# Performance work log

Hardware: AMD Instinct MI355X
Metric: run time of the kernel (lower is better)

Reference implementation:

```python
import jax, jax.numpy as jnp
import numpy as np

N = 100000   # nodes
E = 1600000  # message-passing edges (avg degree 16)
ES = 500000  # scored edges (edge_subgraph)
H = 64       # hidden_features
L = 3        # num_layers
NF = 2       # node_features
EF = 2       # edge_features


def setup_inputs() -> dict:
    key = jax.random.key(0)
    ks = jax.random.split(key, 20)
    s = lambda fan_in: 1.0 / np.sqrt(fan_in)
    inp = {
        "x": jax.random.normal(ks[0], (N, NF), jnp.float32),
        "e": jax.random.normal(ks[1], (E, EF), jnp.float32),
        # encoder linears
        "Wn": jax.random.normal(ks[2], (NF, H), jnp.float32) * s(NF),
        "bn": jnp.zeros((H,), jnp.float32),
        "We": jax.random.normal(ks[3], (EF, H), jnp.float32) * s(EF),
        "be": jnp.zeros((H,), jnp.float32),
        # GatedGCN per-layer weights (stacked over L layers)
        # e' = h_src@A + h_dst@B + e@C + cb ; h' = h@U + sum(sig(e')*h_src@V)/sum(sig(e'))
        "A": jax.random.normal(ks[4], (L, H, H), jnp.float32) * s(H),
        "B": jax.random.normal(ks[5], (L, H, H), jnp.float32) * s(H),
        "C": jax.random.normal(ks[6], (L, H, H), jnp.float32) * s(H),
        "cb": jnp.zeros((L, H), jnp.float32),
        "U": jax.random.normal(ks[7], (L, H, H), jnp.float32) * s(H),
        "V": jax.random.normal(ks[8], (L, H, H), jnp.float32) * s(H),
        # score predictor: Linear(2H, 1)
        "Wp": jax.random.normal(ks[9], (2 * H, 1), jnp.float32) * s(2 * H),
        "bp": jnp.zeros((1,), jnp.float32),
        # graph structure
        "src": jax.random.randint(ks[10], (E,), 0, N, jnp.int32),
        "dst": jax.random.randint(ks[11], (E,), 0, N, jnp.int32),
        "src_s": jax.random.randint(ks[12], (ES,), 0, N, jnp.int32),
        "dst_s": jax.random.randint(ks[13], (ES,), 0, N, jnp.int32),
    }
    return inp


def reference(x, e, Wn, bn, We, be, A, B, C, cb, U, V, Wp, bp, src, dst, src_s, dst_s):
    n = x.shape[0]
    h = x @ Wn + bn          # node encode [N, H]
    e = e @ We + be          # edge encode [E, H]
    for i in range(A.shape[0]):  # fixed small layer loop
        hs = h[src]          # gather src feats [E, H]
        hd = h[dst]          # gather dst feats [E, H]
        e_hat = hs @ A[i] + hd @ B[i] + e @ C[i] + cb[i]
        sigma = jax.nn.sigmoid(e_hat)
        num = jax.ops.segment_sum(sigma * (hs @ V[i]), dst, num_segments=n)
        den = jax.ops.segment_sum(sigma, dst, num_segments=n) + 1e-6
        h = jax.nn.relu(h @ U[i] + num / den)
        e = jax.nn.relu(e_hat)
    # apply_edges: gather-concat-linear on scored edge set
    data = jnp.concatenate([h[src_s], h[dst_s]], axis=1)  # [ES, 2H]
    scores = data @ Wp + bp                               # [ES, 1]
    return scores
```

## Files before the change

### kernel.cpp

```cpp
#include <hip/hip_runtime.h>
#include <hip/hip_bf16.h>

using bf16 = __hip_bfloat16;
typedef __attribute__((ext_vector_type(8))) short short8;
typedef __attribute__((ext_vector_type(4))) float f32x4;
typedef __attribute__((ext_vector_type(4))) int   iv4;

static constexpr int NN = 100000;
static constexpr int NE = 1600000;
static constexpr int NS = 500000;
static constexpr int HH = 64;
static constexpr int SCAN_B = 1024;
static constexpr int SCAN_G = (NN + SCAN_B - 1) / SCAN_B;
static constexpr int DPW = 8;
static constexpr int NGRP = (NN + DPW - 1) / DPW;

__device__ __forceinline__ float b2f(bf16 v) { return __bfloat162float(v); }
__device__ __forceinline__ bf16  f2b(float v) { return __float2bfloat16(v); }
__device__ __forceinline__ float bflo(int u)  { return __uint_as_float(((unsigned)u) << 16); }
__device__ __forceinline__ float bfhi(int u)  { return __uint_as_float(((unsigned)u) & 0xffff0000u); }
__device__ __forceinline__ int pk2(float a, float b) {
    unsigned lo = __bfloat16_as_ushort(__float2bfloat16(a));
    unsigned hi = __bfloat16_as_ushort(__float2bfloat16(b));
    return (int)(lo | (hi << 16));
}
__device__ __forceinline__ int bcasti(int v, int k) {
    return __builtin_amdgcn_readlane(v, k);
}


__global__ void encode_nodes_k(const float* __restrict__ x, const float* __restrict__ Wn,
                               const float* __restrict__ bn, float* __restrict__ h) {
    int tid = blockIdx.x * blockDim.x + threadIdx.x;
    if (tid >= NN * HH) return;
    int r = tid >> 6, j = tid & 63;
    h[tid] = fmaf(x[2 * r], Wn[j], fmaf(x[2 * r + 1], Wn[HH + j], bn[j]));
}

__global__ void prep_k(const float* __restrict__ We, const float* __restrict__ be,
                       const float* __restrict__ C0, const float* __restrict__ cb0,
                       float* __restrict__ We0, float* __restrict__ bb0) {
    int j = threadIdx.x;
    if (j >= HH) return;
    float s0 = 0.f, s1 = 0.f, sb = 0.f;
    for (int k = 0; k < HH; ++k) {
        float c = C0[k * HH + j];
        s0 = fmaf(We[k], c, s0);
        s1 = fmaf(We[HH + k], c, s1);
        sb = fmaf(be[k], c, sb);
    }
    We0[j] = s0; We0[HH + j] = s1; bb0[j] = sb + cb0[j];
}


__global__ void zero_int_k(int* __restrict__ p, int n) {
    int i = blockIdx.x * blockDim.x + threadIdx.x;
    if (i < n) p[i] = 0;
}

__global__ void hist_k(const int* __restrict__ dst, int* __restrict__ cnt) {
    int i = blockIdx.x * blockDim.x + threadIdx.x;
    if (i < NE) atomicAdd(&cnt[dst[i]], 1);
}

__global__ void scan1_k(const int* __restrict__ cnt, int* __restrict__ rowptr,
                        int* __restrict__ bsum) {
    __shared__ int sm[SCAN_B];
    int t = threadIdx.x, idx = blockIdx.x * SCAN_B + t;
    int v = (idx < NN) ? cnt[idx] : 0;
    sm[t] = v;
    __syncthreads();
    for (int off = 1; off < SCAN_B; off <<= 1) {
        int add = (t >= off) ? sm[t - off] : 0;
        __syncthreads();
        sm[t] += add;
        __syncthreads();
    }
    if (idx < NN) rowptr[idx] = sm[t] - v;
    if (t == SCAN_B - 1) bsum[blockIdx.x] = sm[t];
}

__global__ void scan2_k(const int* __restrict__ bsum, int* __restrict__ bofs) {
    if (threadIdx.x == 0) {
        int acc = 0;
        for (int b = 0; b < SCAN_G; ++b) { bofs[b] = acc; acc += bsum[b]; }
    }
}

__global__ void scan3_k(int* __restrict__ rowptr, int* __restrict__ cursor,
                        const int* __restrict__ bofs) {
    int idx = blockIdx.x * SCAN_B + threadIdx.x;
    if (idx < NN) {
        int r = rowptr[idx] + bofs[blockIdx.x];
        rowptr[idx] = r;
        cursor[idx] = r;
    }
    if (idx == 0) rowptr[NN] = NE;
}

__global__ void scatter_k(const int* __restrict__ dst, const int* __restrict__ src,
                          const float2* __restrict__ e0, int* __restrict__ cursor,
                          int4* __restrict__ sedge) {
    int i = blockIdx.x * blockDim.x + threadIdx.x;
    if (i < NE) {
        int p = atomicAdd(&cursor[dst[i]], 1);
        float2 ev = e0[i];
        sedge[p] = make_int4(src[i], __float_as_int(ev.x), __float_as_int(ev.y), 0);
    }
}

__global__ __launch_bounds__(256, 2)
void transform_mfma_k(const float* __restrict__ h,
                      const float* __restrict__ A, const float* __restrict__ B,
                      const float* __restrict__ V, const float* __restrict__ U,
                      bf16* __restrict__ oA, bf16* __restrict__ oB,
                      bf16* __restrict__ oV, bf16* __restrict__ oU) {
    __shared__ __align__(16) char lds_all[4 * 2048];
    char* lds = lds_all + (threadIdx.x >> 6) * 2048;
    const int lane = threadIdx.x & 63;
    const int l15 = lane & 15, lg = lane >> 4, kb = lg * 8;
    const float *W0, *W1; bf16 *o0, *o1;
    if (blockIdx.y == 0) { W0 = A; W1 = B; o0 = oA; o1 = oB; }
    else                 { W0 = V; W1 = U; o0 = oV; o1 = oU; }

    short8 wf[2][4][2];
#pragma unroll
    for (int m = 0; m < 2; ++m) {
        const float* W = m ? W1 : W0;
#pragma unroll
        for (int t = 0; t < 4; ++t)
#pragma unroll
            for (int f = 0; f < 2; ++f) {
                iv4 q;
#pragma unroll
                for (int j = 0; j < 4; ++j)
                    q[j] = pk2(W[(f * 32 + kb + 2 * j) * HH + t * 16 + l15],
                               W[(f * 32 + kb + 2 * j + 1) * HH + t * 16 + l15]);
                __builtin_memcpy(&wf[m][t][f], &q, 16);
            }
    }
    const int sw = (l15 & 7) << 4;
    int wave = blockIdx.x * 4 + (threadIdx.x >> 6);
    int nw = gridDim.x * 4;
    for (int tile = wave; tile < NN / 16; tile += nw) {
        int row0 = tile * 16;
        const float* hr = h + (size_t)(row0 + l15) * HH + kb;
        float4 v0 = *(const float4*)(hr);
        float4 v1 = *(const float4*)(hr + 4);
        float4 v2 = *(const float4*)(hr + 32);
        float4 v3 = *(const float4*)(hr + 36);
        iv4 pa, pb;
        pa[0] = pk2(v0.x, v0.y); pa[1] = pk2(v0.z, v0.w);
        pa[2] = pk2(v1.x, v1.y); pa[3] = pk2(v1.z, v1.w);
        pb[0] = pk2(v2.x, v2.y); pb[1] = pk2(v2.z, v2.w);
        pb[2] = pk2(v3.x, v3.y); pb[3] = pk2(v3.z, v3.w);
        short8 af0, af1;
        __builtin_memcpy(&af0, &pa, 16);
        __builtin_memcpy(&af1, &pb, 16);
#pragma unroll
        for (int m = 0; m < 2; ++m) {
            f32x4 acc[4];
#pragma unroll
            for (int t = 0; t < 4; ++t) acc[t] = f32x4{0.f, 0.f, 0.f, 0.f};
#pragma unroll
            for (int t = 0; t < 4; ++t) {
                acc[t] = __builtin_amdgcn_mfma_f32_16x16x32_bf16(af0, wf[m][t][0], acc[t], 0, 0, 0);
                acc[t] = __builtin_amdgcn_mfma_f32_16x16x32_bf16(af1, wf[m][t][1], acc[t], 0, 0, 0);
            }
#pragma unroll
            for (int t = 0; t < 4; ++t)
#pragma unroll
                for (int r = 0; r < 4; ++r) {
                    int row = lg * 4 + r;
                    int ad = (row * 128 + (t * 16 + l15) * 2) ^ ((row & 7) << 4);
                    *(unsigned short*)(lds + ad) =
                        __bfloat16_as_ushort(__float2bfloat16(acc[t][r]));
                }
            int base = l15 * 128 + lg * 32;
            iv4 q0, q1;
            __builtin_memcpy(&q0, lds + ((base) ^ sw), 16);
            __builtin_memcpy(&q1, lds + ((base + 16) ^ sw), 16);
            bf16* out = m ? o1 : o0;
            *(iv4*)(out + (size_t)(row0 + l15) * HH + lg * 16) = q0;
            *(iv4*)(out + (size_t)(row0 + l15) * HH + lg * 16 + 8) = q1;
        }
    }
}

__global__ __launch_bounds__(256, 2)
void agg0_k(float* __restrict__ h, const bf16* __restrict__ tabs,
            const float* __restrict__ We0, const float* __restrict__ bb0,
            const int* __restrict__ rowptr, const int4* __restrict__ sedge) {
    __shared__ float fl_all[4][128];
    float* fl = fl_all[threadIdx.x >> 6];
    const int lane = threadIdx.x & 63;
    const int l15 = lane & 15, lg = lane >> 4;
    const int f0 = l15 * 4;
    const size_t nb = (size_t)NN * HH;

    float w0f[4], w1f[4], bbf[4];
#pragma unroll
    for (int q = 0; q < 4; ++q) {
        w0f[q] = We0[f0 + q];
        w1f[q] = We0[HH + f0 + q];
        bbf[q] = bb0[f0 + q];
    }

    struct R0 { uint2 a0[4], hv[4]; };
    const int nwaves = gridDim.x * 4;
    for (int g = blockIdx.x * 4 + (threadIdx.x >> 6); g < NGRP; g += nwaves) {
        int dA = g * DPW;
        int ndst = min(DPW, NN - dA);
        int rpv = rowptr[dA + min(lane, ndst)];

        auto endof = [&](int i2) { return bcasti(rpv, i2 + 1); };
        auto begof = [&](int i2) { return bcasti(rpv, i2); };
        auto ldsed = [&](int i2, int b2) -> int4 {
            int en = endof(i2);
            int idx = b2 + min(l15, en - b2 - 1);
            return sedge[idx];
        };
        auto ldrows = [&](const int4& sd, R0& R) {
#pragma unroll
            for (int r = 0; r < 4; ++r) {
                int s = __shfl(sd.x, lg + 4 * r);
                R.a0[r] = *(const uint2*)(tabs + (size_t)s * HH + f0);
                R.hv[r] = *(const uint2*)(tabs + 6 * nb + (size_t)s * HH + f0);
            }
        };
        auto succ = [&](int& i2, int& b2) {
            if (i2 >= ndst) return;
            if (b2 + 16 < endof(i2)) { b2 += 16; return; }
            i2++;
            while (i2 < ndst && endof(i2) <= begof(i2)) i2++;
            if (i2 < ndst) b2 = begof(i2);
        };

        int iC = 0;
        while (iC < ndst && endof(iC) <= begof(iC)) iC++;
        int bC = (iC < ndst) ? begof(iC) : 0;
        int4 sedC = make_int4(0, 0, 0, 0), sedN = sedC;
        R0 rowsC, rowsN;
        if (iC < ndst) sedC = ldsed(iC, bC);
        int iN = iC, bN = bC;
        if (iC < ndst) succ(iN, bN);
        if (iN < ndst) sedN = ldsed(iN, bN);
        if (iC < ndst) ldrows(sedC, rowsC);

        for (int i = 0; i < ndst; ++i) {
            size_t drow = (size_t)(dA + i) * HH;
            float hu = b2f(tabs[7 * nb + drow + lane]);
            float zb[4];
            {
                uint2 bv = *(const uint2*)(tabs + nb + drow + f0);
                zb[0] = bbf[0] + bflo(bv.x); zb[1] = bbf[1] + bfhi(bv.x);
                zb[2] = bbf[2] + bflo(bv.y); zb[3] = bbf[3] + bfhi(bv.y);
            }
            float nm[4] = {0.f, 0.f, 0.f, 0.f}, dn[4] = {0.f, 0.f, 0.f, 0.f};

            while (iC == i) {
                if (iN < ndst) ldrows(sedN, rowsN);
                int iF = iN, bF = bN;
                succ(iF, bF);
                int4 sedF = sedN;
                if (iF < ndst) sedF = ldsed(iF, bF);

                int cnt = min(endof(i) - bC, 16);
#pragma unroll
                for (int r = 0; r < 4; ++r) {
                    int s = lg + 4 * r;
                    bool valid = s < cnt;
                    float ex = __int_as_float(__shfl(sedC.y, s));
                    float ey = __int_as_float(__shfl(sedC.z, s));
                    uint2 a0 = rowsC.a0[r], hv = rowsC.hv[r];
                    float av[4] = {bflo(a0.x), bfhi(a0.x), bflo(a0.y), bfhi(a0.y)};
                    float hvv[4] = {bflo(hv.x), bfhi(hv.x), bflo(hv.y), bfhi(hv.y)};
#pragma unroll
                    for (int q = 0; q < 4; ++q) {
                        float z = fmaf(ex, w0f[q], fmaf(ey, w1f[q], zb[q])) + av[q];
                        float sg = valid ? 1.f / (1.f + __expf(-z)) : 0.f;
                        nm[q] = fmaf(sg, hvv[q], nm[q]);
                        dn[q] += sg;
                    }
                }
                sedC = sedN; rowsC = rowsN; iC = iN; bC = bN;
                iN = iF; bN = bF; sedN = sedF;
            }

#pragma unroll
            for (int m = 16; m < 64; m <<= 1)
#pragma unroll
                for (int q = 0; q < 4; ++q) {
                    nm[q] += __shfl_xor(nm[q], m);
                    dn[q] += __shfl_xor(dn[q], m);
                }
            if (lg == 0) {
#pragma unroll
                for (int q = 0; q < 4; ++q) {
                    fl[f0 + q] = nm[q];
                    fl[64 + f0 + q] = dn[q];
                }
            }
            float nmv = fl[lane], dnv = fl[64 + lane];
            h[drow + lane] = fmaxf(hu + nmv / (dnv + 1e-6f), 0.f);
        }
    }
}

struct Rows { iv4 ra, rb, hva, hvb, b1a, b1b, b2a, b2b; };

template <int LAYER>
__global__ __launch_bounds__(256, 2)
void agg_k(float* __restrict__ h, const bf16* __restrict__ tabs,
           const float* __restrict__ We0, const float* __restrict__ bb0,
           const float* __restrict__ cb, const float* __restrict__ C,
           const int* __restrict__ rowptr, const int4* __restrict__ sedge) {
    __shared__ __align__(16) char cfr[LAYER >= 2 ? 16384 : 8192];
    constexpr int WLDS = (LAYER == 1 ? 4096 : 6144);
    __shared__ __align__(16) char lds_all[4 * WLDS];
    char* lds = lds_all + (threadIdx.x >> 6) * WLDS;
    char* Lb1 = lds;
    char* Lb2 = lds + 2048;
    char* Lhv = lds + (LAYER >= 2 ? 4096 : 2048);
    char* Le1 = lds;
    const int lane = threadIdx.x & 63;
    const int l15 = lane & 15, lg = lane >> 4, kb = lg * 8;
    const size_t nb = (size_t)NN * HH;

    {
        int t = threadIdx.x >> 6;
        const float* C1 = C + 1 * HH * HH;
        const float* C2 = C + 2 * HH * HH;
#pragma unroll
        for (int f = 0; f < 2; ++f) {
            iv4 q;
#pragma unroll
            for (int j = 0; j < 4; ++j)
                q[j] = pk2(C1[(f * 32 + kb + 2 * j) * HH + t * 16 + l15],
                           C1[(f * 32 + kb + 2 * j + 1) * HH + t * 16 + l15]);
            *(iv4*)(cfr + ((t * 2 + f) * 64 + lane) * 16) = q;
            if constexpr (LAYER >= 2) {
                iv4 p;
#pragma unroll
                for (int j = 0; j < 4; ++j)
                    p[j] = pk2(C2[(f * 32 + kb + 2 * j) * HH + t * 16 + l15],
                               C2[(f * 32 + kb + 2 * j + 1) * HH + t * 16 + l15]);
                *(iv4*)(cfr + 8192 + ((t * 2 + f) * 64 + lane) * 16) = p;
            }
        }
        __syncthreads();
    }

    float w0a[8], w0b[8], w1a[8], w1b[8], bba[8], bbb[8];
#pragma unroll
    for (int j = 0; j < 8; ++j) {
        w0a[j] = We0[kb + j];        w0b[j] = We0[32 + kb + j];
        w1a[j] = We0[HH + kb + j];   w1b[j] = We0[HH + 32 + kb + j];
        bba[j] = bb0[kb + j];        bbb[j] = bb0[32 + kb + j];
    }
    float cb1t[4], cb2t[4];
#pragma unroll
    for (int t = 0; t < 4; ++t) cb1t[t] = cb[HH + t * 16 + l15];
    if constexpr (LAYER >= 2) {
#pragma unroll
        for (int t = 0; t < 4; ++t) cb2t[t] = cb[2 * HH + t * 16 + l15];
    }
    const int wlo = (l15 * 128 + lg * 16) ^ ((l15 & 7) << 4);
    const int whi = (l15 * 128 + 64 + lg * 16) ^ ((l15 & 7) << 4);

    const int nwaves = gridDim.x * 4;
    for (int g = blockIdx.x * 4 + (threadIdx.x >> 6); g < NGRP; g += nwaves) {
        int dA = g * DPW;
        int ndst = min(DPW, NN - dA);
        int rpv = rowptr[dA + min(lane, ndst)];

        auto endof = [&](int i2) { return bcasti(rpv, i2 + 1); };
        auto begof = [&](int i2) { return bcasti(rpv, i2); };
        auto ldsed = [&](int i2, int b2) -> int4 {
            int en = endof(i2);
            int idx = b2 + min(l15, en - b2 - 1);
            return sedge[idx];
        };
        auto ldrows = [&](const int4& sd, Rows& R) {
            size_t srow = (size_t)sd.x * HH;
            R.ra  = *(const iv4*)(tabs + srow + kb);
            R.rb  = *(const iv4*)(tabs + srow + 32 + kb);
            R.hva = *(const iv4*)(tabs + 6 * nb + srow + kb);
            R.hvb = *(const iv4*)(tabs + 6 * nb + srow + 32 + kb);
            R.b1a = *(const iv4*)(tabs + 2 * nb + srow + kb);
            R.b1b = *(const iv4*)(tabs + 2 * nb + srow + 32 + kb);
            if constexpr (LAYER >= 2) {
                R.b2a = *(const iv4*)(tabs + 4 * nb + srow + kb);
                R.b2b = *(const iv4*)(tabs + 4 * nb + srow + 32 + kb);
            }
        };
        auto succ = [&](int& i2, int& b2) {
            if (i2 >= ndst) return;
            if (b2 + 16 < endof(i2)) { b2 += 16; return; }
            i2++;
            while (i2 < ndst && endof(i2) <= begof(i2)) i2++;
            if (i2 < ndst) b2 = begof(i2);
        };

        int iC = 0;
        while (iC < ndst && endof(iC) <= begof(iC)) iC++;
        int bC = (iC < ndst) ? begof(iC) : 0;
        int4 sedC = make_int4(0, 0, 0, 0), sedN = sedC;
        Rows rowsC, rowsN;
        if (iC < ndst) sedC = ldsed(iC, bC);
        int iN = iC, bN = bC;
        if (iC < ndst) succ(iN, bN);
        if (iN < ndst) sedN = ldsed(iN, bN);
        if (iC < ndst) ldrows(sedC, rowsC);

        for (int i = 0; i < ndst; ++i) {
            size_t drow = (size_t)(dA + i) * HH;
            float hu = b2f(tabs[7 * nb + drow + lane]);
            float zba[8], zbb[8];
            {
                iv4 ba  = *(const iv4*)(tabs + nb + drow + kb);
                iv4 bbv = *(const iv4*)(tabs + nb + drow + 32 + kb);
#pragma unroll
                for (int q = 0; q < 4; ++q) {
                    zba[2 * q]     = bba[2 * q]     + bflo(ba[q]);
                    zba[2 * q + 1] = bba[2 * q + 1] + bfhi(ba[q]);
                    zbb[2 * q]     = bbb[2 * q]     + bflo(bbv[q]);
                    zbb[2 * q + 1] = bbb[2 * q + 1] + bfhi(bbv[q]);
                }
            }
            float c1d[4], c2d[4];
#pragma unroll
            for (int t = 0; t < 4; ++t)
                c1d[t] = cb1t[t] + b2f(tabs[3 * nb + drow + t * 16 + l15]);
            if constexpr (LAYER >= 2) {
#pragma unroll
                for (int t = 0; t < 4; ++t)
                    c2d[t] = cb2t[t] + b2f(tabs[5 * nb + drow + t * 16 + l15]);
            }

            float nmT[4] = {0.f, 0.f, 0.f, 0.f}, dnT[4] = {0.f, 0.f, 0.f, 0.f};

            while (iC == i) {
                if (iN < ndst) ldrows(sedN, rowsN);
                int iF = iN, bF = bN;
                succ(iF, bF);
                int4 sedF = sedN;
                if (iF < ndst) sedF = ldsed(iF, bF);

                int cnt = min(endof(i) - bC, 16);
                float ex = __int_as_float(sedC.y), ey = __int_as_float(sedC.z);
                float za[8], zc[8];
#pragma unroll
                for (int q = 0; q < 4; ++q) {
                    za[2*q]   = fmaf(ex, w0a[2*q],   fmaf(ey, w1a[2*q],   zba[2*q]))   + bflo(rowsC.ra[q]);
                    za[2*q+1] = fmaf(ex, w0a[2*q+1], fmaf(ey, w1a[2*q+1], zba[2*q+1])) + bfhi(rowsC.ra[q]);
                    zc[2*q]   = fmaf(ex, w0b[2*q],   fmaf(ey, w1b[2*q],   zbb[2*q]))   + bflo(rowsC.rb[q]);
                    zc[2*q+1] = fmaf(ex, w0b[2*q+1], fmaf(ey, w1b[2*q+1], zbb[2*q+1])) + bfhi(rowsC.rb[q]);
                }
                *(iv4*)(Lhv + wlo) = rowsC.hva;  *(iv4*)(Lhv + whi) = rowsC.hvb;
                *(iv4*)(Lb1 + wlo) = rowsC.b1a;  *(iv4*)(Lb1 + whi) = rowsC.b1b;
                if constexpr (LAYER >= 2) {
                    *(iv4*)(Lb2 + wlo) = rowsC.b2a;  *(iv4*)(Lb2 + whi) = rowsC.b2b;
                }
                iv4 pa, pb;
#pragma unroll
                for (int q = 0; q < 4; ++q) {
                    pa[q] = pk2(fmaxf(za[2*q], 0.f), fmaxf(za[2*q+1], 0.f));
                    pb[q] = pk2(fmaxf(zc[2*q], 0.f), fmaxf(zc[2*q+1], 0.f));
                }
                short8 af0, af1;
                __builtin_memcpy(&af0, &pa, 16);
                __builtin_memcpy(&af1, &pb, 16);
                f32x4 acc[4];
#pragma unroll
                for (int t = 0; t < 4; ++t) {
                    f32x4 a;
#pragma unroll
                    for (int r = 0; r < 4; ++r) {
                        int row = lg * 4 + r;
                        int ad = (row * 128 + (t * 16 + l15) * 2) ^ ((row & 7) << 4);
                        a[r] = c1d[t] + b2f(*(const bf16*)(Lb1 + ad));
                    }
                    acc[t] = a;
                }
                __builtin_amdgcn_s_setprio(1);
#pragma unroll
                for (int t = 0; t < 4; ++t) {
                    short8 q0, q1;
                    __builtin_memcpy(&q0, cfr + ((t * 2 + 0) * 64 + lane) * 16, 16);
                    __builtin_memcpy(&q1, cfr + ((t * 2 + 1) * 64 + lane) * 16, 16);
                    acc[t] = __builtin_amdgcn_mfma_f32_16x16x32_bf16(af0, q0, acc[t], 0, 0, 0);
                    acc[t] = __builtin_amdgcn_mfma_f32_16x16x32_bf16(af1, q1, acc[t], 0, 0, 0);
                }
                __builtin_amdgcn_s_setprio(0);
                if constexpr (LAYER >= 2) {
#pragma unroll
                    for (int t = 0; t < 4; ++t)
#pragma unroll
                        for (int r = 0; r < 4; ++r) {
                            int row = lg * 4 + r;
                            int ad = (row * 128 + (t * 16 + l15) * 2) ^ ((row & 7) << 4);
                            *(unsigned short*)(Le1 + ad) =
                                __bfloat16_as_ushort(__float2bfloat16(fmaxf(acc[t][r], 0.f)));
                        }
                    short8 ag0, ag1;
                    __builtin_memcpy(&ag0, Le1 + ((l15 * 128 + kb * 2) ^ ((l15 & 7) << 4)), 16);
                    __builtin_memcpy(&ag1, Le1 + ((l15 * 128 + 64 + kb * 2) ^ ((l15 & 7) << 4)), 16);
#pragma unroll
                    for (int t = 0; t < 4; ++t) {
                        f32x4 a;
#pragma unroll
                        for (int r = 0; r < 4; ++r) {
                            int row = lg * 4 + r;
                            int ad = (row * 128 + (t * 16 + l15) * 2) ^ ((row & 7) << 4);
                            a[r] = c2d[t] + b2f(*(const bf16*)(Lb2 + ad));
                        }
                        acc[t] = a;
                    }
                    __builtin_amdgcn_s_setprio(1);
#pragma unroll
                    for (int t = 0; t < 4; ++t) {
                        short8 q0, q1;
                        __builtin_memcpy(&q0, cfr + 8192 + ((t * 2 + 0) * 64 + lane) * 16, 16);
                        __builtin_memcpy(&q1, cfr + 8192 + ((t * 2 + 1) * 64 + lane) * 16, 16);
                        acc[t] = __builtin_amdgcn_mfma_f32_16x16x32_bf16(ag0, q0, acc[t], 0, 0, 0);
                        acc[t] = __builtin_amdgcn_mfma_f32_16x16x32_bf16(ag1, q1, acc[t], 0, 0, 0);
                    }
                    __builtin_amdgcn_s_setprio(0);
                }
#pragma unroll
                for (int r = 0; r < 4; ++r) {
                    int row = lg * 4 + r;
                    bool valid = row < cnt;
#pragma unroll
                    for (int t = 0; t < 4; ++t) {
                        float sg = valid ? 1.f / (1.f + __expf(-acc[t][r])) : 0.f;
                        int ad = (row * 128 + (t * 16 + l15) * 2) ^ ((row & 7) << 4);
                        nmT[t] = fmaf(sg, b2f(*(const bf16*)(Lhv + ad)), nmT[t]);
                        dnT[t] += sg;
                    }
                }
                sedC = sedN; rowsC = rowsN; iC = iN; bC = bN;
                iN = iF; bN = bF; sedN = sedF;
            }

            float* fl = (float*)Le1;
#pragma unroll
            for (int m = 16; m < 64; m <<= 1)
#pragma unroll
                for (int t = 0; t < 4; ++t) {
                    nmT[t] += __shfl_xor(nmT[t], m);
                    dnT[t] += __shfl_xor(dnT[t], m);
                }
            if (lg == 0) {
#pragma unroll
                for (int t = 0; t < 4; ++t) {
                    fl[t * 16 + l15]      = nmT[t];
                    fl[64 + t * 16 + l15] = dnT[t];
                }
            }
            float nmv = fl[lane], dnv = fl[64 + lane];
            h[drow + lane] = fmaxf(hu + nmv / (dnv + 1e-6f), 0.f);
        }
    }
}

__global__ void prescore_k(const float* __restrict__ h, const float* __restrict__ Wp,
                           float* __restrict__ ps, float* __restrict__ pd) {
    int lane = threadIdx.x & 63;
    int wave = blockIdx.x * (blockDim.x >> 6) + (threadIdx.x >> 6);
    int nw = gridDim.x * (blockDim.x >> 6);
    float wa = Wp[lane], wb = Wp[HH + lane];
    for (int r = wave; r < NN; r += nw) {
        float hv = h[(size_t)r * HH + lane];
        float a = hv * wa, b = hv * wb;
#pragma unroll
        for (int off = 32; off; off >>= 1) {
            a += __shfl_xor(a, off);
            b += __shfl_xor(b, off);
        }
        if (lane == 0) { ps[r] = a; pd[r] = b; }
    }
}

__global__ void score2_k(const float* __restrict__ ps, const float* __restrict__ pd,
                         const float* __restrict__ bp, const int* __restrict__ ss,
                         const int* __restrict__ ds, float* __restrict__ out) {
    int i = blockIdx.x * blockDim.x + threadIdx.x;
    if (i < NS) out[i] = ps[ss[i]] + pd[ds[i]] + bp[0];
}

extern "C" void kernel_launch(void* const* d_in, const int* in_sizes, int n_in,
                              void* d_out, int out_size, void* d_ws, size_t ws_size,
                              hipStream_t stream) {
    const float* x  = (const float*)d_in[0];
    const float* e0 = (const float*)d_in[1];
    const float* Wn = (const float*)d_in[2];
    const float* bn = (const float*)d_in[3];
    const float* We = (const float*)d_in[4];
    const float* be = (const float*)d_in[5];
    const float* A  = (const float*)d_in[6];
    const float* B  = (const float*)d_in[7];
    const float* C  = (const float*)d_in[8];
    const float* cb = (const float*)d_in[9];
    const float* U  = (const float*)d_in[10];
    const float* V  = (const float*)d_in[11];
    const float* Wp = (const float*)d_in[12];
    const float* bp = (const float*)d_in[13];
    const int* src  = (const int*)d_in[14];
    const int* dst  = (const int*)d_in[15];
    const int* ss   = (const int*)d_in[16];
    const int* ds   = (const int*)d_in[17];

    char* ws = (char*)d_ws;
    size_t nb = (size_t)NN * HH;
    float* h      = (float*)ws;
    bf16*  tabs   = (bf16*)(ws + nb * 4);
    int4*  sedge  = (int4*)(tabs + 8 * nb);
    int*   cnt    = (int*)(sedge + NE);
    int*   rowptr = cnt + NN;
    int*   cursor = rowptr + (NN + 1);
    int*   bsum   = cursor + NN;
    int*   bofs   = bsum + SCAN_G;
    float* We0    = (float*)(bofs + SCAN_G);
    float* bb0    = We0 + 2 * HH;
    float* ps     = bb0 + HH;
    float* pd     = ps + NN;

    encode_nodes_k<<<(NN * HH + 255) / 256, 256, 0, stream>>>(x, Wn, bn, h);
    prep_k<<<1, 64, 0, stream>>>(We, be, C, cb, We0, bb0);

    zero_int_k<<<(NN + 255) / 256, 256, 0, stream>>>(cnt, NN);
    hist_k<<<(NE + 255) / 256, 256, 0, stream>>>(dst, cnt);
    scan1_k<<<SCAN_G, SCAN_B, 0, stream>>>(cnt, rowptr, bsum);
    scan2_k<<<1, 64, 0, stream>>>(bsum, bofs);
    scan3_k<<<SCAN_G, SCAN_B, 0, stream>>>(rowptr, cursor, bofs);
    scatter_k<<<(NE + 255) / 256, 256, 0, stream>>>(dst, src, (const float2*)e0,
                                                    cursor, sedge);

    for (int l = 0; l < 3; ++l) {
        transform_mfma_k<<<dim3(128, 2), 256, 0, stream>>>(
            h, A + (size_t)l * HH * HH, B + (size_t)l * HH * HH,
            V + (size_t)l * HH * HH, U + (size_t)l * HH * HH,
            tabs + 2 * (size_t)l * nb, tabs + (2 * (size_t)l + 1) * nb,
            tabs + 6 * nb, tabs + 7 * nb);
        if (l == 0)
            agg0_k<<<1024, 256, 0, stream>>>(h, tabs, We0, bb0, rowptr, sedge);
        else if (l == 1)
            agg_k<1><<<1024, 256, 0, stream>>>(h, tabs, We0, bb0, cb, C, rowptr, sedge);
        else
            agg_k<2><<<1024, 256, 0, stream>>>(h, tabs, We0, bb0, cb, C, rowptr, sedge);
    }

    prescore_k<<<512, 256, 0, stream>>>(h, Wp, ps, pd);
    score2_k<<<(NS + 255) / 256, 256, 0, stream>>>(ps, pd, bp, ss, ds, (float*)d_out);
}
```

Measured before the change: 953.0 us.

## Fuse node encoder and score projection into layers, add dynamic work queue

The node encoder is folded into the first transform kernel, which now computes h from x, Wn and bn on the fly instead of reading a materialized h. The final aggregation layer computes the per-node score projections directly, which removes the prescore kernel and the last write and read of h. Aggregation kernels take work groups from an atomic counter instead of a static stride, and the group size drops from 8 to 4 destinations to balance uneven degrees. The cost is one atomic per group and more, smaller groups.

```diff
diff --git a/kernel.cpp b/kernel.cpp
--- a/kernel.cpp
+++ b/kernel.cpp
@@ -12,11 +12,10 @@
 static constexpr int HH = 64;
 static constexpr int SCAN_B = 1024;
 static constexpr int SCAN_G = (NN + SCAN_B - 1) / SCAN_B;
-static constexpr int DPW = 8;
+static constexpr int DPW = 4;
 static constexpr int NGRP = (NN + DPW - 1) / DPW;
 
 __device__ __forceinline__ float b2f(bf16 v) { return __bfloat162float(v); }
-__device__ __forceinline__ bf16  f2b(float v) { return __float2bfloat16(v); }
 __device__ __forceinline__ float bflo(int u)  { return __uint_as_float(((unsigned)u) << 16); }
 __device__ __forceinline__ float bfhi(int u)  { return __uint_as_float(((unsigned)u) & 0xffff0000u); }
 __device__ __forceinline__ int pk2(float a, float b) {
@@ -28,14 +27,6 @@
     return __builtin_amdgcn_readlane(v, k);
 }
 
-
-__global__ void encode_nodes_k(const float* __restrict__ x, const float* __restrict__ Wn,
-                               const float* __restrict__ bn, float* __restrict__ h) {
-    int tid = blockIdx.x * blockDim.x + threadIdx.x;
-    if (tid >= NN * HH) return;
-    int r = tid >> 6, j = tid & 63;
-    h[tid] = fmaf(x[2 * r], Wn[j], fmaf(x[2 * r + 1], Wn[HH + j], bn[j]));
-}
 
 __global__ void prep_k(const float* __restrict__ We, const float* __restrict__ be,
                        const float* __restrict__ C0, const float* __restrict__ cb0,
@@ -109,8 +100,10 @@
     }
 }
 
+template <bool FIRST>
 __global__ __launch_bounds__(256, 2)
-void transform_mfma_k(const float* __restrict__ h,
+void transform_mfma_k(const float* __restrict__ h, const float* __restrict__ x,
+                      const float* __restrict__ Wn, const float* __restrict__ bn,
                       const float* __restrict__ A, const float* __restrict__ B,
                       const float* __restrict__ V, const float* __restrict__ U,
                       bf16* __restrict__ oA, bf16* __restrict__ oB,
@@ -144,16 +137,29 @@
     int nw = gridDim.x * 4;
     for (int tile = wave; tile < NN / 16; tile += nw) {
         int row0 = tile * 16;
-        const float* hr = h + (size_t)(row0 + l15) * HH + kb;
-        float4 v0 = *(const float4*)(hr);
-        float4 v1 = *(const float4*)(hr + 4);
-        float4 v2 = *(const float4*)(hr + 32);
-        float4 v3 = *(const float4*)(hr + 36);
         iv4 pa, pb;
-        pa[0] = pk2(v0.x, v0.y); pa[1] = pk2(v0.z, v0.w);
-        pa[2] = pk2(v1.x, v1.y); pa[3] = pk2(v1.z, v1.w);
-        pb[0] = pk2(v2.x, v2.y); pb[1] = pk2(v2.z, v2.w);
-        pb[2] = pk2(v3.x, v3.y); pb[3] = pk2(v3.z, v3.w);
+        if constexpr (FIRST) {
+            float2 xv = *(const float2*)(x + 2 * (size_t)(row0 + l15));
+#pragma unroll
+            for (int j = 0; j < 4; ++j) {
+                int k0 = kb + 2 * j;
+                pa[j] = pk2(fmaf(xv.x, Wn[k0],     fmaf(xv.y, Wn[HH + k0],     bn[k0])),
+                            fmaf(xv.x, Wn[k0 + 1], fmaf(xv.y, Wn[HH + k0 + 1], bn[k0 + 1])));
+                int k1 = 32 + kb + 2 * j;
+                pb[j] = pk2(fmaf(xv.x, Wn[k1],     fmaf(xv.y, Wn[HH + k1],     bn[k1])),
+                            fmaf(xv.x, Wn[k1 + 1], fmaf(xv.y, Wn[HH + k1 + 1], bn[k1 + 1])));
+            }
+        } else {
+            const float* hr = h + (size_t)(row0 + l15) * HH + kb;
+            float4 v0 = *(const float4*)(hr);
+            float4 v1 = *(const float4*)(hr + 4);
+            float4 v2 = *(const float4*)(hr + 32);
+            float4 v3 = *(const float4*)(hr + 36);
+            pa[0] = pk2(v0.x, v0.y); pa[1] = pk2(v0.z, v0.w);
+            pa[2] = pk2(v1.x, v1.y); pa[3] = pk2(v1.z, v1.w);
+            pb[0] = pk2(v2.x, v2.y); pb[1] = pk2(v2.z, v2.w);
+            pb[2] = pk2(v3.x, v3.y); pb[3] = pk2(v3.z, v3.w);
+        }
         short8 af0, af1;
         __builtin_memcpy(&af0, &pa, 16);
         __builtin_memcpy(&af1, &pb, 16);
@@ -190,7 +196,8 @@
 __global__ __launch_bounds__(256, 2)
 void agg0_k(float* __restrict__ h, const bf16* __restrict__ tabs,
             const float* __restrict__ We0, const float* __restrict__ bb0,
-            const int* __restrict__ rowptr, const int4* __restrict__ sedge) {
+            const int* __restrict__ rowptr, const int4* __restrict__ sedge,
+            int* __restrict__ wq) {
     __shared__ float fl_all[4][128];
     float* fl = fl_all[threadIdx.x >> 6];
     const int lane = threadIdx.x & 63;
@@ -207,8 +214,11 @@
     }
 
     struct R0 { uint2 a0[4], hv[4]; };
-    const int nwaves = gridDim.x * 4;
-    for (int g = blockIdx.x * 4 + (threadIdx.x >> 6); g < NGRP; g += nwaves) {
+    for (;;) {
+        int g0 = 0;
+        if (lane == 0) g0 = atomicAdd(wq, 1);
+        int g = __builtin_amdgcn_readfirstlane(g0);
+        if (g >= NGRP) break;
         int dA = g * DPW;
         int ndst = min(DPW, NN - dA);
         int rpv = rowptr[dA + min(lane, ndst)];
@@ -314,7 +324,9 @@
 void agg_k(float* __restrict__ h, const bf16* __restrict__ tabs,
            const float* __restrict__ We0, const float* __restrict__ bb0,
            const float* __restrict__ cb, const float* __restrict__ C,
-           const int* __restrict__ rowptr, const int4* __restrict__ sedge) {
+           const int* __restrict__ rowptr, const int4* __restrict__ sedge,
+           int* __restrict__ wq, const float* __restrict__ Wp,
+           float* __restrict__ ps, float* __restrict__ pd) {
     __shared__ __align__(16) char cfr[LAYER >= 2 ? 16384 : 8192];
     constexpr int WLDS = (LAYER == 1 ? 4096 : 6144);
     __shared__ __align__(16) char lds_all[4 * WLDS];
@@ -365,11 +377,16 @@
 #pragma unroll
         for (int t = 0; t < 4; ++t) cb2t[t] = cb[2 * HH + t * 16 + l15];
     }
+    float wpa = 0.f, wpb = 0.f;
+    if constexpr (LAYER >= 2) { wpa = Wp[lane]; wpb = Wp[HH + lane]; }
     const int wlo = (l15 * 128 + lg * 16) ^ ((l15 & 7) << 4);
     const int whi = (l15 * 128 + 64 + lg * 16) ^ ((l15 & 7) << 4);
 
-    const int nwaves = gridDim.x * 4;
-    for (int g = blockIdx.x * 4 + (threadIdx.x >> 6); g < NGRP; g += nwaves) {
+    for (;;) {
+        int g0 = 0;
+        if (lane == 0) g0 = atomicAdd(wq, 1);
+        int g = __builtin_amdgcn_readfirstlane(g0);
+        if (g >= NGRP) break;
         int dA = g * DPW;
         int ndst = min(DPW, NN - dA);
         int rpv = rowptr[dA + min(lane, ndst)];
@@ -560,26 +577,19 @@
                 }
             }
             float nmv = fl[lane], dnv = fl[64 + lane];
-            h[drow + lane] = fmaxf(hu + nmv / (dnv + 1e-6f), 0.f);
+            float hval = fmaxf(hu + nmv / (dnv + 1e-6f), 0.f);
+            if constexpr (LAYER < 2) {
+                h[drow + lane] = hval;
+            } else {
+                float a = hval * wpa, b = hval * wpb;
+#pragma unroll
+                for (int m = 32; m; m >>= 1) {
+                    a += __shfl_xor(a, m);
+                    b += __shfl_xor(b, m);
+                }
+                if (lane == 0) { ps[dA + i] = a; pd[dA + i] = b; }
+            }
         }
-    }
-}
-
-__global__ void prescore_k(const float* __restrict__ h, const float* __restrict__ Wp,
-                           float* __restrict__ ps, float* __restrict__ pd) {
-    int lane = threadIdx.x & 63;
-    int wave = blockIdx.x * (blockDim.x >> 6) + (threadIdx.x >> 6);
-    int nw = gridDim.x * (blockDim.x >> 6);
-    float wa = Wp[lane], wb = Wp[HH + lane];
-    for (int r = wave; r < NN; r += nw) {
-        float hv = h[(size_t)r * HH + lane];
-        float a = hv * wa, b = hv * wb;
-#pragma unroll
-        for (int off = 32; off; off >>= 1) {
-            a += __shfl_xor(a, off);
-            b += __shfl_xor(b, off);
-        }
-        if (lane == 0) { ps[r] = a; pd[r] = b; }
     }
 }
 
@@ -626,11 +636,12 @@
     float* bb0    = We0 + 2 * HH;
     float* ps     = bb0 + HH;
     float* pd     = ps + NN;
-
-    encode_nodes_k<<<(NN * HH + 255) / 256, 256, 0, stream>>>(x, Wn, bn, h);
+    int*   wq     = (int*)(pd + NN);
+
     prep_k<<<1, 64, 0, stream>>>(We, be, C, cb, We0, bb0);
 
     zero_int_k<<<(NN + 255) / 256, 256, 0, stream>>>(cnt, NN);
+    zero_int_k<<<1, 64, 0, stream>>>(wq, 4);
     hist_k<<<(NE + 255) / 256, 256, 0, stream>>>(dst, cnt);
     scan1_k<<<SCAN_G, SCAN_B, 0, stream>>>(cnt, rowptr, bsum);
     scan2_k<<<1, 64, 0, stream>>>(bsum, bofs);
@@ -639,19 +650,29 @@
                                                     cursor, sedge);
 
     for (int l = 0; l < 3; ++l) {
-        transform_mfma_k<<<dim3(128, 2), 256, 0, stream>>>(
-            h, A + (size_t)l * HH * HH, B + (size_t)l * HH * HH,
-            V + (size_t)l * HH * HH, U + (size_t)l * HH * HH,
-            tabs + 2 * (size_t)l * nb, tabs + (2 * (size_t)l + 1) * nb,
-            tabs + 6 * nb, tabs + 7 * nb);
         if (l == 0)
-            agg0_k<<<1024, 256, 0, stream>>>(h, tabs, We0, bb0, rowptr, sedge);
+            transform_mfma_k<true><<<dim3(128, 2), 256, 0, stream>>>(
+                h, x, Wn, bn,
+                A + (size_t)l * HH * HH, B + (size_t)l * HH * HH,
+                V + (size_t)l * HH * HH, U + (size_t)l * HH * HH,
+                tabs + 2 * (size_t)l * nb, tabs + (2 * (size_t)l + 1) * nb,
+                tabs + 6 * nb, tabs + 7 * nb);
+        else
+            transform_mfma_k<false><<<dim3(128, 2), 256, 0, stream>>>(
+                h, x, Wn, bn,
+                A + (size_t)l * HH * HH, B + (size_t)l * HH * HH,
+                V + (size_t)l * HH * HH, U + (size_t)l * HH * HH,
+                tabs + 2 * (size_t)l * nb, tabs + (2 * (size_t)l + 1) * nb,
+                tabs + 6 * nb, tabs + 7 * nb);
+        if (l == 0)
+            agg0_k<<<1024, 256, 0, stream>>>(h, tabs, We0, bb0, rowptr, sedge, wq + 0);
         else if (l == 1)
-            agg_k<1><<<1024, 256, 0, stream>>>(h, tabs, We0, bb0, cb, C, rowptr, sedge);
+            agg_k<1><<<1024, 256, 0, stream>>>(h, tabs, We0, bb0, cb, C, rowptr, sedge,
+                                               wq + 1, Wp, ps, pd);
         else
-            agg_k<2><<<1024, 256, 0, stream>>>(h, tabs, We0, bb0, cb, C, rowptr, sedge);
-    }
-
-    prescore_k<<<512, 256, 0, stream>>>(h, Wp, ps, pd);
+            agg_k<2><<<1024, 256, 0, stream>>>(h, tabs, We0, bb0, cb, C, rowptr, sedge,
+                                               wq + 2, Wp, ps, pd);
+    }
+
     score2_k<<<(NS + 255) / 256, 256, 0, stream>>>(ps, pd, bp, ss, ds, (float*)d_out);
 }
```

Measured after the change: 1.379 ms. +44.6%, slower.
